# Kernel optimization log

Measured on AMD Instinct MI355X. Metric: run time of the kernel, lower is better.

Reference implementation:

```python
import jax, jax.numpy as jnp
import numpy as np

N_NODES = 100000
N_EDGES = 3200000
ALPHA = 0.1
ITERATIONS = 10


def setup_inputs() -> dict:
    key = jax.random.key(0)
    ks = jax.random.split(key, 7)
    features = jax.random.normal(ks[0], (N_NODES, 512), dtype=jnp.float32)
    W1 = jax.random.normal(ks[1], (512, 64), dtype=jnp.float32) * 0.05
    b1 = jax.random.normal(ks[2], (64,), dtype=jnp.float32) * 0.05
    W2 = jax.random.normal(ks[3], (64, 64), dtype=jnp.float32) * 0.05
    b2 = jax.random.normal(ks[4], (64,), dtype=jnp.float32) * 0.05
    edge_weights = jax.random.uniform(ks[5], (N_EDGES,), dtype=jnp.float32)
    edge_index = jax.random.randint(ks[6], (2, N_EDGES), 0, N_NODES, dtype=jnp.int64)
    return {"features": features, "W1": W1, "b1": b1, "W2": W2, "b2": b2,
            "edge_weights": edge_weights, "edge_index": edge_index}


def reference(features, W1, b1, W2, b2, edge_weights, edge_index):
    # dense MLP head (dropout disabled / eval mode)
    h = jax.nn.relu(features @ W1 + b1)          # [N, hidden]
    z = h @ W2 + b2                              # [N, labels]

    row, col = edge_index[0], edge_index[1]

    def step(p, _):
        # SpMM: out[row] += w * p[col]
        gathered = edge_weights[:, None] * p[col]                 # [E, labels]
        new = jax.ops.segment_sum(gathered, row, num_segments=N_NODES)
        p = (1.0 - ALPHA) * new + ALPHA * z
        return p, None

    p, _ = jax.lax.scan(step, z, None, length=ITERATIONS)
    return p
```

## Files before the change

kernel.cpp:

```cpp
#include <hip/hip_runtime.h>
#include <hip/hip_fp16.h>
#include <cmath>

#define N_NODES 100000
#define N_EDGES 3200000
#define ALPHA   0.1f
#define ITERS   10
#define NBUK    1024
#define RPB     98
#define CHUNK   8192
#define NCH     391

typedef __attribute__((ext_vector_type(8))) short short8;
typedef __attribute__((ext_vector_type(4))) float f32x4;

__device__ __forceinline__ short f2bf(float x) {
    union { float f; unsigned u; } v; v.f = x;
    unsigned r = v.u + 0x7fffu + ((v.u >> 16) & 1u);
    return (short)(r >> 16);
}

__global__ void prep_w(const float* __restrict__ W1, const float* __restrict__ W2,
                       short* __restrict__ W1t, short* __restrict__ W2t)
{
    int t = blockIdx.x * 256 + threadIdx.x;
    if (t < 512 * 64) { int k = t >> 6, c = t & 63; W1t[c * 512 + k] = f2bf(W1[t]); }
    if (t < 64 * 64)  { int k = t >> 6, c = t & 63; W2t[c * 64 + k]  = f2bf(W2[t]); }
}

__global__ __launch_bounds__(128) void mlp_mfma(
    const float* __restrict__ F, const short* __restrict__ W1t,
    const short* __restrict__ W2t, const float* __restrict__ b1,
    const float* __restrict__ b2, __half* __restrict__ q0)
{
    __shared__ short Ft[32 * 128];
    __shared__ short Ht[32 * 64];

    const int t  = threadIdx.x;
    const int l  = t & 63;
    const int wv = t >> 6;
    const int wr = wv * 16;
    const long base = (long)blockIdx.x * 32;

    const int sr = t >> 2;
    const int ck = (t & 3) * 32;

    float4 f0, f1, f2, f3, f4, f5, f6, f7;

#define LOAD_TILE(kt) do {                                                   \
    const float* p_ = F + (base + sr) * 512 + (kt) * 128 + ck;               \
    f0 = *(const float4*)(p_ +  0);  f1 = *(const float4*)(p_ +  4);         \
    f2 = *(const float4*)(p_ +  8);  f3 = *(const float4*)(p_ + 12);         \
    f4 = *(const float4*)(p_ + 16);  f5 = *(const float4*)(p_ + 20);         \
    f6 = *(const float4*)(p_ + 24);  f7 = *(const float4*)(p_ + 28);         \
} while (0)

#define STORE_PAIR(j2, fa, fb) do {                                          \
    int k_ = ck + (j2) * 8;                                                  \
    short8 s_ = { f2bf((fa).x), f2bf((fa).y), f2bf((fa).z), f2bf((fa).w),    \
                  f2bf((fb).x), f2bf((fb).y), f2bf((fb).z), f2bf((fb).w) };  \
    *(short8*)&Ft[(sr * 128 + k_) ^ ((sr & 7) << 3)] = s_;                   \
} while (0)

    LOAD_TILE(0);

    f32x4 acc[4] = {};
    for (int kt = 0; kt < 4; ++kt) {
        STORE_PAIR(0, f0, f1);
        STORE_PAIR(1, f2, f3);
        STORE_PAIR(2, f4, f5);
        STORE_PAIR(3, f6, f7);
        __syncthreads();
        if (kt < 3) LOAD_TILE(kt + 1);
#pragma unroll
        for (int kc = 0; kc < 4; ++kc) {
            int kb = kc * 32 + (l >> 4) * 8;
            int ar = wr + (l & 15);
            short8 a = *(const short8*)&Ft[(ar * 128 + kb) ^ ((ar & 7) << 3)];
#pragma unroll
            for (int n = 0; n < 4; ++n) {
                int bc = n * 16 + (l & 15);
                short8 b = *(const short8*)(W1t + bc * 512 + kt * 128 + kb);
                acc[n] = __builtin_amdgcn_mfma_f32_16x16x32_bf16(a, b, acc[n], 0, 0, 0);
            }
        }
        __syncthreads();
    }

#pragma unroll
    for (int n = 0; n < 4; ++n) {
        int col = n * 16 + (l & 15);
        float bv = b1[col];
#pragma unroll
        for (int i = 0; i < 4; ++i) {
            int row = wr + (l >> 4) * 4 + i;
            float hv = fmaxf(acc[n][i] + bv, 0.0f);
            Ht[(row * 64 + col) ^ ((row & 7) << 3)] = f2bf(hv);
        }
    }
    f32x4 acc2[4] = {};
#pragma unroll
    for (int kc = 0; kc < 2; ++kc) {
        int kb = kc * 32 + (l >> 4) * 8;
        int ar = wr + (l & 15);
        short8 a = *(const short8*)&Ht[(ar * 64 + kb) ^ ((ar & 7) << 3)];
#pragma unroll
        for (int n = 0; n < 4; ++n) {
            int bc = n * 16 + (l & 15);
            short8 b = *(const short8*)(W2t + bc * 64 + kb);
            acc2[n] = __builtin_amdgcn_mfma_f32_16x16x32_bf16(a, b, acc2[n], 0, 0, 0);
        }
    }
#pragma unroll
    for (int n = 0; n < 4; ++n) {
        int col = n * 16 + (l & 15);
        float bv = b2[col];
#pragma unroll
        for (int i = 0; i < 4; ++i) {
            long row = base + wr + (l >> 4) * 4 + i;
            q0[row * 64 + col] = __float2half(acc2[n][i] + bv);
        }
    }
#undef LOAD_TILE
#undef STORE_PAIR
}

__global__ __launch_bounds__(256) void bhist(const int* __restrict__ rows, int* __restrict__ gh)
{
    __shared__ int cnt[NBUK];
    for (int i = threadIdx.x; i < NBUK; i += 256) cnt[i] = 0;
    __syncthreads();
    int base = blockIdx.x * CHUNK;
    int end  = base + CHUNK; if (end > N_EDGES) end = N_EDGES;
    for (int i = base + threadIdx.x; i < end; i += 256)
        atomicAdd(&cnt[rows[i] / RPB], 1);
    __syncthreads();
    for (int i = threadIdx.x; i < NBUK; i += 256)
        gh[i * NCH + blockIdx.x] = cnt[i];
}

__global__ __launch_bounds__(512) void bscan(int* __restrict__ gh, int* __restrict__ btot)
{
    __shared__ int s[512];
    int k = blockIdx.x;
    int t = threadIdx.x;
    int v = (t < NCH) ? gh[k * NCH + t] : 0;
    s[t] = v;
    __syncthreads();
    for (int off = 1; off < 512; off <<= 1) {
        int x = (t >= off) ? s[t - off] : 0;
        __syncthreads();
        s[t] += x;
        __syncthreads();
    }
    if (t < NCH) gh[k * NCH + t] = s[t] - v;
    if (t == NCH - 1) btot[k] = s[t];
}

__global__ __launch_bounds__(1024) void scan_btot(const int* __restrict__ btot, int* __restrict__ bbase)
{
    __shared__ int s[1024];
    int t = threadIdx.x;
    int v = btot[t];
    s[t] = v;
    __syncthreads();
    for (int off = 1; off < 1024; off <<= 1) {
        int x = (t >= off) ? s[t - off] : 0;
        __syncthreads();
        s[t] += x;
        __syncthreads();
    }
    bbase[t] = s[t] - v;
}

__global__ __launch_bounds__(256) void bpart(const int* __restrict__ rows, const int* __restrict__ cols,
                                             const float* __restrict__ w, const int* __restrict__ gh,
                                             const int* __restrict__ bbase, uint2* __restrict__ stg)
{
    __shared__ int cur[NBUK];
    int blk = blockIdx.x;
    for (int i = threadIdx.x; i < NBUK; i += 256)
        cur[i] = bbase[i] + gh[i * NCH + blk];
    __syncthreads();
    int base = blk * CHUNK;
    int end  = base + CHUNK; if (end > N_EDGES) end = N_EDGES;
    for (int i = base + threadIdx.x; i < end; i += 256) {
        int r = rows[i];
        int b = r / RPB;
        int pos = atomicAdd(&cur[b], 1);
        float ws = w[i] * ((1.0f - ALPHA) / 16.0f);
        unsigned meta = (unsigned)cols[i] | ((unsigned)(r - b * RPB) << 17);
        stg[pos] = make_uint2(meta, __float_as_uint(ws));
    }
}

__global__ __launch_bounds__(256) void bucket_sort2(const int* __restrict__ bbase,
                                                    const uint2* __restrict__ stg,
                                                    unsigned* __restrict__ cw,
                                                    int* __restrict__ rowp)
{
    __shared__ int ldeg[RPB];
    __shared__ int lcur[RPB];
    __shared__ int sc[128];
    const int b = blockIdx.x;
    const int rowlo = b * RPB;
    if (rowlo >= N_NODES) return;
    int rowhi = rowlo + RPB; if (rowhi > N_NODES) rowhi = N_NODES;
    const int nrows = rowhi - rowlo;
    const int t = threadIdx.x;
    const int base = bbase[b];
    const int cnt = ((b + 1 < NBUK) ? bbase[b + 1] : N_EDGES) - base;

    if (t < RPB) ldeg[t] = 0;
    __syncthreads();
    for (int j = t; j < cnt; j += 256)
        atomicAdd(&ldeg[stg[base + j].x >> 17], 1);
    __syncthreads();
    int v = 0;
    if (t < 128) { v = (t < nrows) ? ldeg[t] : 0; sc[t] = v; }
    __syncthreads();
    for (int off = 1; off < 128; off <<= 1) {
        int x = (t < 128 && t >= off) ? sc[t - off] : 0;
        __syncthreads();
        if (t < 128) sc[t] += x;
        __syncthreads();
    }
    if (t < nrows) {
        int rp = base + sc[t] - v;
        rowp[rowlo + t] = rp;
        lcur[t] = rp;
    }
    if (t == 0 && rowhi == N_NODES) rowp[N_NODES] = base + cnt;
    __syncthreads();
    for (int j = t; j < cnt; j += 256) {
        uint2 rec = stg[base + j];
        int roff = rec.x >> 17;
        unsigned col = rec.x & 0x1FFFFu;
        int pos = atomicAdd(&lcur[roff], 1);
        unsigned short hb = __half_as_ushort(__float2half(__uint_as_float(rec.y)));
        cw[pos] = col | ((unsigned)hb << 17);
    }
}

template <int LAST>
__global__ __launch_bounds__(256) void spmm_kernel(
    const int* __restrict__ rowp, const unsigned* __restrict__ cw,
    const __half* __restrict__ qin, const __half* __restrict__ zh,
    float beta, float outscale,
    __half* __restrict__ qout, float* __restrict__ out)
{
    const int wid = blockIdx.x * 4 + (threadIdx.x >> 6);
    if (wid >= N_NODES) return;
    const int lane = threadIdx.x & 63;
    const int sub  = lane >> 3;
    const int l8   = lane & 7;

    const int start = rowp[wid];
    const int end   = rowp[wid + 1];

    uint4 zv = *(const uint4*)(zh + (long)wid * 64 + l8 * 8);

    float a0 = 0, a1 = 0, a2 = 0, a3 = 0, a4 = 0, a5 = 0, a6 = 0, a7 = 0;

#define ACC_EDGE(pc, v)                                                       \
    do {                                                                      \
        float ww_ = __half2float(__ushort_as_half((unsigned short)((pc) >> 17))); \
        float2 p_;                                                            \
        p_ = __half22float2(*(__half2*)&(v).x); a0 += ww_ * p_.x; a1 += ww_ * p_.y; \
        p_ = __half22float2(*(__half2*)&(v).y); a2 += ww_ * p_.x; a3 += ww_ * p_.y; \
        p_ = __half22float2(*(__half2*)&(v).z); a4 += ww_ * p_.x; a5 += ww_ * p_.y; \
        p_ = __half22float2(*(__half2*)&(v).w); a6 += ww_ * p_.x; a7 += ww_ * p_.y; \
    } while (0)

    int e = start + sub;
    for (; e + 8 < end; e += 16) {
        unsigned pc0 = cw[e];
        unsigned pc1 = cw[e + 8];
        uint4 v0 = *(const uint4*)(qin + (long)(pc0 & 0x1FFFFu) * 64 + l8 * 8);
        uint4 v1 = *(const uint4*)(qin + (long)(pc1 & 0x1FFFFu) * 64 + l8 * 8);
        ACC_EDGE(pc0, v0);
        ACC_EDGE(pc1, v1);
    }
    if (e < end) {
        unsigned pc = cw[e];
        uint4 v = *(const uint4*)(qin + (long)(pc & 0x1FFFFu) * 64 + l8 * 8);
        ACC_EDGE(pc, v);
    }
#undef ACC_EDGE

    a0 += __shfl_xor(a0, 8);  a1 += __shfl_xor(a1, 8);
    a2 += __shfl_xor(a2, 8);  a3 += __shfl_xor(a3, 8);
    a4 += __shfl_xor(a4, 8);  a5 += __shfl_xor(a5, 8);
    a6 += __shfl_xor(a6, 8);  a7 += __shfl_xor(a7, 8);
    a0 += __shfl_xor(a0, 16); a1 += __shfl_xor(a1, 16);
    a2 += __shfl_xor(a2, 16); a3 += __shfl_xor(a3, 16);
    a4 += __shfl_xor(a4, 16); a5 += __shfl_xor(a5, 16);
    a6 += __shfl_xor(a6, 16); a7 += __shfl_xor(a7, 16);
    a0 += __shfl_xor(a0, 32); a1 += __shfl_xor(a1, 32);
    a2 += __shfl_xor(a2, 32); a3 += __shfl_xor(a3, 32);
    a4 += __shfl_xor(a4, 32); a5 += __shfl_xor(a5, 32);
    a6 += __shfl_xor(a6, 32); a7 += __shfl_xor(a7, 32);

    if (lane < 8) {
        float2 z0 = __half22float2(*(__half2*)&zv.x);
        float2 z1 = __half22float2(*(__half2*)&zv.y);
        float2 z2 = __half22float2(*(__half2*)&zv.z);
        float2 z3 = __half22float2(*(__half2*)&zv.w);
        float o0 = a0 + beta * z0.x, o1 = a1 + beta * z0.y;
        float o2 = a2 + beta * z1.x, o3 = a3 + beta * z1.y;
        float o4 = a4 + beta * z2.x, o5 = a5 + beta * z2.y;
        float o6 = a6 + beta * z3.x, o7 = a7 + beta * z3.y;
        if (LAST) {
            float4 ra = { outscale * o0, outscale * o1, outscale * o2, outscale * o3 };
            float4 rb = { outscale * o4, outscale * o5, outscale * o6, outscale * o7 };
            *(float4*)(out + (long)wid * 64 + lane * 8)     = ra;
            *(float4*)(out + (long)wid * 64 + lane * 8 + 4) = rb;
        } else {
            __half2 h0 = __floats2half2_rn(o0, o1);
            __half2 h1 = __floats2half2_rn(o2, o3);
            __half2 h2 = __floats2half2_rn(o4, o5);
            __half2 h3 = __floats2half2_rn(o6, o7);
            uint4 pv = { *(unsigned*)&h0, *(unsigned*)&h1, *(unsigned*)&h2, *(unsigned*)&h3 };
            *(uint4*)(qout + (long)wid * 64 + lane * 8) = pv;
        }
    }
}

extern "C" void kernel_launch(void* const* d_in, const int* in_sizes, int n_in,
                              void* d_out, int out_size, void* d_ws, size_t ws_size,
                              hipStream_t stream)
{
    const float* features = (const float*)d_in[0];
    const float* W1 = (const float*)d_in[1];
    const float* b1 = (const float*)d_in[2];
    const float* W2 = (const float*)d_in[3];
    const float* b2 = (const float*)d_in[4];
    const float* ew = (const float*)d_in[5];
    const int*   ei = (const int*)d_in[6];
    const int* erow = ei;
    const int* ecol = ei + N_EDGES;
    float* out = (float*)d_out;

    char* ws = (char*)d_ws;
    size_t off = 0;
    auto alloc = [&](size_t bytes) {
        size_t c = off;
        off += (bytes + 255) & ~(size_t)255;
        return c;
    };
    __half* q0    = (__half*)(ws + alloc((size_t)N_NODES * 64 * 2));
    __half* qA    = (__half*)(ws + alloc((size_t)N_NODES * 64 * 2));
    __half* qB    = (__half*)(ws + alloc((size_t)N_NODES * 64 * 2));
    unsigned* cw  = (unsigned*)(ws + alloc((size_t)N_EDGES * 4));
    uint2* stg    = (uint2*)(ws + alloc((size_t)N_EDGES * 8));
    int*   gh     = (int*)  (ws + alloc((size_t)NBUK * NCH * 4));
    short* W1t    = (short*)(ws + alloc((size_t)512 * 64 * 2));
    short* W2t    = (short*)(ws + alloc((size_t)64 * 64 * 2));
    int*   rowp   = (int*)  (ws + alloc((size_t)(N_NODES + 1) * 4));
    int*   btot   = (int*)  (ws + alloc((size_t)NBUK * 4));
    int*   bbase  = (int*)  (ws + alloc((size_t)NBUK * 4));
    (void)ws_size; (void)in_sizes; (void)n_in; (void)out_size;

    prep_w<<<128, 256, 0, stream>>>(W1, W2, W1t, W2t);
    mlp_mfma<<<N_NODES / 32, 128, 0, stream>>>(features, W1t, W2t, b1, b2, q0);

    bhist<<<NCH, 256, 0, stream>>>(erow, gh);
    bscan<<<NBUK, 512, 0, stream>>>(gh, btot);
    scan_btot<<<1, 1024, 0, stream>>>(btot, bbase);
    bpart<<<NCH, 256, 0, stream>>>(erow, ecol, ew, gh, bbase, stg);
    bucket_sort2<<<NBUK, 256, 0, stream>>>(bbase, stg, cw, rowp);

    const __half* qi = q0;
    for (int it = 1; it < ITERS; ++it) {
        __half* qo = (it & 1) ? qA : qB;
        float beta = (float)(0.1 / pow(16.0, (double)it));
        spmm_kernel<0><<<(N_NODES + 3) / 4, 256, 0, stream>>>(rowp, cw, qi, q0, beta, 1.0f, qo, nullptr);
        qi = qo;
    }
    float beta10 = (float)(0.1 / pow(16.0, 10.0));
    float osc    = (float)pow(16.0, 10.0);
    spmm_kernel<1><<<(N_NODES + 3) / 4, 256, 0, stream>>>(rowp, cw, qi, q0, beta10, osc, nullptr, out);
}
```

Baseline: 745.2 us.

## Split feature matrix into four 16-column planes for cache-friendly SpMM gathers

Stores the propagated fp16 feature matrix as four column planes of 16 features each instead of row-major 64-wide rows. The SpMM launches four times as many blocks, each handling one plane, and each wave gathers 8-byte chunks for 16 edges at once. A single plane (about 3.2 MB) fits in L2/LLC far better than the full 12.8 MB matrix, which is meant to cut DRAM traffic from the random gathers. In exchange, the CSR column/weight stream and row pointers are read four times per iteration, and the gathers become narrower, 8-byte accesses.

Measured after the change: 1.395 ms. +87.2%, slower.

```diff
diff --git a/kernel.cpp b/kernel.cpp
--- a/kernel.cpp
+++ b/kernel.cpp
@@ -10,6 +10,7 @@
 #define RPB     98
 #define CHUNK   8192
 #define NCH     391
+#define PLANE   ((size_t)N_NODES * 16)
 
 typedef __attribute__((ext_vector_type(8))) short short8;
 typedef __attribute__((ext_vector_type(4))) float f32x4;
@@ -113,12 +114,11 @@
     }
 #pragma unroll
     for (int n = 0; n < 4; ++n) {
-        int col = n * 16 + (l & 15);
-        float bv = b2[col];
+        float bv = b2[n * 16 + (l & 15)];
 #pragma unroll
         for (int i = 0; i < 4; ++i) {
             long row = base + wr + (l >> 4) * 4 + i;
-            q0[row * 64 + col] = __float2half(acc2[n][i] + bv);
+            q0[(size_t)n * PLANE + row * 16 + (l & 15)] = __float2half(acc2[n][i] + bv);
         }
     }
 #undef LOAD_TILE
@@ -249,18 +249,20 @@
     float beta, float outscale,
     __half* __restrict__ qout, float* __restrict__ out)
 {
-    const int wid = blockIdx.x * 4 + (threadIdx.x >> 6);
-    if (wid >= N_NODES) return;
+    const int g   = blockIdx.x / 25000;
+    const int wid = (blockIdx.x % 25000) * 4 + (threadIdx.x >> 6);
     const int lane = threadIdx.x & 63;
-    const int sub  = lane >> 3;
-    const int l8   = lane & 7;
+    const int slot = lane >> 2;
+    const int l4   = lane & 3;
+
+    const __half* qg = qin + (size_t)g * PLANE;
 
     const int start = rowp[wid];
     const int end   = rowp[wid + 1];
 
-    uint4 zv = *(const uint4*)(zh + (long)wid * 64 + l8 * 8);
-
-    float a0 = 0, a1 = 0, a2 = 0, a3 = 0, a4 = 0, a5 = 0, a6 = 0, a7 = 0;
+    uint2 zv = *(const uint2*)(zh + (size_t)g * PLANE + wid * 16 + l4 * 4);
+
+    float a0 = 0, a1 = 0, a2 = 0, a3 = 0;
 
 #define ACC_EDGE(pc, v)                                                       \
     do {                                                                      \
@@ -268,60 +270,46 @@
         float2 p_;                                                            \
         p_ = __half22float2(*(__half2*)&(v).x); a0 += ww_ * p_.x; a1 += ww_ * p_.y; \
         p_ = __half22float2(*(__half2*)&(v).y); a2 += ww_ * p_.x; a3 += ww_ * p_.y; \
-        p_ = __half22float2(*(__half2*)&(v).z); a4 += ww_ * p_.x; a5 += ww_ * p_.y; \
-        p_ = __half22float2(*(__half2*)&(v).w); a6 += ww_ * p_.x; a7 += ww_ * p_.y; \
     } while (0)
 
-    int e = start + sub;
-    for (; e + 8 < end; e += 16) {
+    int e = start + slot;
+    for (; e + 16 < end; e += 32) {
         unsigned pc0 = cw[e];
-        unsigned pc1 = cw[e + 8];
-        uint4 v0 = *(const uint4*)(qin + (long)(pc0 & 0x1FFFFu) * 64 + l8 * 8);
-        uint4 v1 = *(const uint4*)(qin + (long)(pc1 & 0x1FFFFu) * 64 + l8 * 8);
+        unsigned pc1 = cw[e + 16];
+        uint2 v0 = *(const uint2*)(qg + (size_t)(pc0 & 0x1FFFFu) * 16 + l4 * 4);
+        uint2 v1 = *(const uint2*)(qg + (size_t)(pc1 & 0x1FFFFu) * 16 + l4 * 4);
         ACC_EDGE(pc0, v0);
         ACC_EDGE(pc1, v1);
     }
     if (e < end) {
         unsigned pc = cw[e];
-        uint4 v = *(const uint4*)(qin + (long)(pc & 0x1FFFFu) * 64 + l8 * 8);
+        uint2 v = *(const uint2*)(qg + (size_t)(pc & 0x1FFFFu) * 16 + l4 * 4);
         ACC_EDGE(pc, v);
     }
 #undef ACC_EDGE
 
+    a0 += __shfl_xor(a0, 4);  a1 += __shfl_xor(a1, 4);
+    a2 += __shfl_xor(a2, 4);  a3 += __shfl_xor(a3, 4);
     a0 += __shfl_xor(a0, 8);  a1 += __shfl_xor(a1, 8);
     a2 += __shfl_xor(a2, 8);  a3 += __shfl_xor(a3, 8);
-    a4 += __shfl_xor(a4, 8);  a5 += __shfl_xor(a5, 8);
-    a6 += __shfl_xor(a6, 8);  a7 += __shfl_xor(a7, 8);
     a0 += __shfl_xor(a0, 16); a1 += __shfl_xor(a1, 16);
     a2 += __shfl_xor(a2, 16); a3 += __shfl_xor(a3, 16);
-    a4 += __shfl_xor(a4, 16); a5 += __shfl_xor(a5, 16);
-    a6 += __shfl_xor(a6, 16); a7 += __shfl_xor(a7, 16);
     a0 += __shfl_xor(a0, 32); a1 += __shfl_xor(a1, 32);
     a2 += __shfl_xor(a2, 32); a3 += __shfl_xor(a3, 32);
-    a4 += __shfl_xor(a4, 32); a5 += __shfl_xor(a5, 32);
-    a6 += __shfl_xor(a6, 32); a7 += __shfl_xor(a7, 32);
-
-    if (lane < 8) {
+
+    if (lane < 4) {
         float2 z0 = __half22float2(*(__half2*)&zv.x);
         float2 z1 = __half22float2(*(__half2*)&zv.y);
-        float2 z2 = __half22float2(*(__half2*)&zv.z);
-        float2 z3 = __half22float2(*(__half2*)&zv.w);
         float o0 = a0 + beta * z0.x, o1 = a1 + beta * z0.y;
         float o2 = a2 + beta * z1.x, o3 = a3 + beta * z1.y;
-        float o4 = a4 + beta * z2.x, o5 = a5 + beta * z2.y;
-        float o6 = a6 + beta * z3.x, o7 = a7 + beta * z3.y;
         if (LAST) {
-            float4 ra = { outscale * o0, outscale * o1, outscale * o2, outscale * o3 };
-            float4 rb = { outscale * o4, outscale * o5, outscale * o6, outscale * o7 };
-            *(float4*)(out + (long)wid * 64 + lane * 8)     = ra;
-            *(float4*)(out + (long)wid * 64 + lane * 8 + 4) = rb;
+            float4 r = { outscale * o0, outscale * o1, outscale * o2, outscale * o3 };
+            *(float4*)(out + (size_t)wid * 64 + g * 16 + lane * 4) = r;
         } else {
             __half2 h0 = __floats2half2_rn(o0, o1);
             __half2 h1 = __floats2half2_rn(o2, o3);
-            __half2 h2 = __floats2half2_rn(o4, o5);
-            __half2 h3 = __floats2half2_rn(o6, o7);
-            uint4 pv = { *(unsigned*)&h0, *(unsigned*)&h1, *(unsigned*)&h2, *(unsigned*)&h3 };
-            *(uint4*)(qout + (long)wid * 64 + lane * 8) = pv;
+            uint2 pv = { *(unsigned*)&h0, *(unsigned*)&h1 };
+            *(uint2*)(qout + (size_t)g * PLANE + wid * 16 + lane * 4) = pv;
         }
     }
 }
@@ -374,10 +362,10 @@
     for (int it = 1; it < ITERS; ++it) {
         __half* qo = (it & 1) ? qA : qB;
         float beta = (float)(0.1 / pow(16.0, (double)it));
-        spmm_kernel<0><<<(N_NODES + 3) / 4, 256, 0, stream>>>(rowp, cw, qi, q0, beta, 1.0f, qo, nullptr);
+        spmm_kernel<0><<<100000, 256, 0, stream>>>(rowp, cw, qi, q0, beta, 1.0f, qo, nullptr);
         qi = qo;
     }
     float beta10 = (float)(0.1 / pow(16.0, 10.0));
     float osc    = (float)pow(16.0, 10.0);
-    spmm_kernel<1><<<(N_NODES + 3) / 4, 256, 0, stream>>>(rowp, cw, qi, q0, beta10, osc, nullptr, out);
-}
+    spmm_kernel<1><<<100000, 256, 0, stream>>>(rowp, cw, qi, q0, beta10, osc, nullptr, out);
+}
```
